# Optimization experiments

Hardware: AMD Instinct MI355X
Metric: run time of the kernel (lower is better)

The kernel has to match this reference:

```python
import jax, jax.numpy as jnp
import numpy as np

D_MODEL = 1024
N_HEADS = 16
FACTOR = 2
KEY_DIM = D_MODEL // N_HEADS            # 64
HEAD_DIM = D_MODEL * FACTOR // N_HEADS  # 128
SCALING = KEY_DIM ** -0.5
BSZ, SEQ = 2, 2048


def _rel_pos(slen):
    # angle: 1/10000**linspace(0,1,key_dim//2), each value repeated twice
    half = jnp.asarray(1.0) / jnp.power(10000.0, jnp.linspace(0.0, 1.0, KEY_DIM // 2))
    angle = jnp.repeat(half, 2)                              # [key_dim]
    decay = jnp.log(1.0 - 2.0 ** (-5.0 - jnp.arange(N_HEADS, dtype=jnp.float32)))  # [h], negative
    idx = jnp.arange(slen, dtype=jnp.float32)
    sin = jnp.sin(idx[:, None] * angle[None, :])             # [s, key_dim]
    cos = jnp.cos(idx[:, None] * angle[None, :])
    diff = idx[:, None] - idx[None, :]                       # [s, s]
    tril = diff >= 0
    mask = jnp.where(tril[None], jnp.exp(diff[None] * decay[:, None, None]), 0.0)  # [h, s, s]
    mask = mask / jnp.sqrt(mask.sum(axis=-1, keepdims=True))
    return sin, cos, mask


def _rotate_every_two(x):
    x1 = x[..., ::2]
    x2 = x[..., 1::2]
    return jnp.stack((-x2, x1), axis=-1).reshape(x.shape)


def _theta_shift(x, sin, cos):
    return x * cos + _rotate_every_two(x) * sin


def setup_inputs() -> dict:
    key = jax.random.key(0)
    ks = jax.random.split(key, 11)
    s = 1.0 / np.sqrt(D_MODEL)
    s2 = 1.0 / np.sqrt(D_MODEL * FACTOR)
    return {
        "x": jax.random.normal(ks[0], (BSZ, SEQ, D_MODEL), jnp.float32),
        "q_w": jax.random.uniform(ks[1], (D_MODEL, D_MODEL), jnp.float32, -s, s),
        "q_b": jax.random.uniform(ks[2], (D_MODEL,), jnp.float32, -s, s),
        "k_w": jax.random.uniform(ks[3], (D_MODEL, D_MODEL), jnp.float32, -s, s),
        "k_b": jax.random.uniform(ks[4], (D_MODEL,), jnp.float32, -s, s),
        "v_w": jax.random.uniform(ks[5], (D_MODEL, D_MODEL * FACTOR), jnp.float32, -s, s),
        "v_b": jax.random.uniform(ks[6], (D_MODEL * FACTOR,), jnp.float32, -s, s),
        "g_w": jax.random.uniform(ks[7], (D_MODEL, D_MODEL * FACTOR), jnp.float32, -s, s),
        "g_b": jax.random.uniform(ks[8], (D_MODEL * FACTOR,), jnp.float32, -s, s),
        "o_w": jax.random.uniform(ks[9], (D_MODEL * FACTOR, D_MODEL), jnp.float32, -s2, s2),
        "o_b": jax.random.uniform(ks[10], (D_MODEL,), jnp.float32, -s2, s2),
    }


def _forward(x, q_w, q_b, k_w, k_b, v_w, v_b, g_w, g_b, o_w, o_b):
    bsz, slen, _ = x.shape
    sin, cos, mask = _rel_pos(slen)
    q = x @ q_w + q_b
    k = (x @ k_w + k_b) * SCALING
    v = x @ v_w + v_b
    g = x @ g_w + g_b
    # [b, h, s, key_dim]
    q = q.reshape(bsz, slen, N_HEADS, KEY_DIM).transpose(0, 2, 1, 3)
    k = k.reshape(bsz, slen, N_HEADS, KEY_DIM).transpose(0, 2, 1, 3)
    qr = _theta_shift(q, sin, cos)
    kr = _theta_shift(k, sin, cos)
    vr = v.reshape(bsz, slen, N_HEADS, HEAD_DIM).transpose(0, 2, 1, 3)  # [b,h,s,head_dim]
    qk = jnp.einsum('bhmd,bhnd->bhmn', qr, kr) * mask                  # decay-masked scores
    denom = jnp.clip(jnp.abs(jax.lax.stop_gradient(qk).sum(axis=-1, keepdims=True)), 1.0, None)
    qk = qk / denom
    out = jnp.einsum('bhmn,bhnd->bhmd', qk, vr).transpose(0, 2, 1, 3)  # [b,s,h,head_dim]
    # per-head LayerNorm over head_dim, no affine
    mu = out.mean(axis=-1, keepdims=True)
    var = out.var(axis=-1, keepdims=True)
    out = (out - mu) / jnp.sqrt(var + 1e-5)
    out = out.reshape(bsz, slen, N_HEADS * HEAD_DIM)
    out = jax.nn.silu(g) * out
    return out @ o_w + o_b


def reference(x, q_w, q_b, k_w, k_b, v_w, v_b, g_w, g_b, o_w, o_b):
    return _forward(x, q_w, q_b, k_w, k_b, v_w, v_b, g_w, g_b, o_w, o_b)
```

## Files before the change

kernel.cpp:

```cpp
#include <hip/hip_runtime.h>
#include <hip/hip_bf16.h>


typedef __hip_bfloat16 bf16;
typedef short bf16x4 __attribute__((ext_vector_type(4)));
typedef short bf16x8 __attribute__((ext_vector_type(8)));
typedef float floatx4 __attribute__((ext_vector_type(4)));

#define B_SZ 2
#define SEQ 2048
#define NH 16
#define KD 64
#define HD 128

#define ASYNC16(gp, lp)                                                             \
  __builtin_amdgcn_global_load_lds(                                                 \
      (const __attribute__((address_space(1))) unsigned int*)(unsigned long long)(const void*)(gp), \
      (__attribute__((address_space(3))) unsigned int*)(unsigned int)(unsigned long long)(void*)(lp), \
      16, 0, 0)

__device__ __forceinline__ float b2f(bf16 x) { return __bfloat162float(x); }
__device__ __forceinline__ bf16 f2b(float x) { return __float2bfloat16(x); }

#define MFMA16(a, bb, c) __builtin_amdgcn_mfma_f32_16x16x32_bf16(a, bb, c, 0, 0, 0)

__global__ void convert_k(const float* __restrict__ in, bf16* __restrict__ out) {
  int i = blockIdx.x * 256 + threadIdx.x;
  float4 v = reinterpret_cast<const float4*>(in)[i];
  union { bf16 h[4]; bf16x4 v4; } u;
  u.h[0] = f2b(v.x); u.h[1] = f2b(v.y); u.h[2] = f2b(v.z); u.h[3] = f2b(v.w);
  reinterpret_cast<bf16x4*>(out)[i] = u.v4;
}

__global__ void transpose_k(const float* __restrict__ in, bf16* __restrict__ out,
                            int K, int N) {
  __shared__ float tile[32][33];
  int tx = threadIdx.x, ty = threadIdx.y;
  int n0 = blockIdx.x * 32, k0 = blockIdx.y * 32;
#pragma unroll
  for (int j = 0; j < 4; ++j)
    tile[ty + j * 8][tx] = in[(size_t)(k0 + ty + j * 8) * N + n0 + tx];
  __syncthreads();
#pragma unroll
  for (int j = 0; j < 4; ++j)
    out[(size_t)(n0 + ty + j * 8) * K + k0 + tx] = f2b(tile[tx][ty + j * 8]);
}

__global__ void vtrans_k(const bf16* __restrict__ in, bf16* __restrict__ out) {
  __shared__ bf16 tile[32][72];
  int tx = threadIdx.x, ty = threadIdx.y;
  int s0 = blockIdx.x * 32, c0 = blockIdx.y * 64, bz = blockIdx.z;
  const bf16* src = in + (size_t)bz * 2048 * 2048;
#pragma unroll
  for (int j = 0; j < 4; ++j) {
    int sr = ty + j * 8;
    tile[sr][tx] = src[(size_t)(s0 + sr) * 2048 + c0 + tx];
    tile[sr][tx + 32] = src[(size_t)(s0 + sr) * 2048 + c0 + 32 + tx];
  }
  __syncthreads();
  int tid = ty * 32 + tx;
  int dl = tid & 63, srun = tid >> 6;
  int c = c0 + dl, hh = c >> 7, d = c & 127;
  int dt = d >> 4, lw = d & 15;
  union { bf16 e[8]; bf16x8 v; } pk;
#pragma unroll
  for (int k = 0; k < 8; ++k) pk.e[k] = tile[srun * 8 + k][dl];
  size_t bh = (size_t)bz * NH + hh;
  int nt = s0 >> 5;
  size_t idx = ((bh * 64 + nt) * 8 + dt) * 512 + (size_t)(srun * 16 + lw) * 8;
  *(bf16x8*)&out[idx] = pk.v;
}

template <int BM, int BN, int KDIM, int MODE>
__global__ __launch_bounds__(256, 2) void gemm_bt(
    const bf16* __restrict__ A, const bf16* __restrict__ Bt, int Ndim,
    const float* __restrict__ bias_q, const float* __restrict__ bias_k,
    const float* __restrict__ bias_v, const float* __restrict__ bias_g,
    float* __restrict__ outCqk, bf16* __restrict__ out_v,
    float* __restrict__ out_g, float* __restrict__ outF) {
  __shared__ bf16 As[BM * 32];
  __shared__ bf16 Bs[BN * 32];
  const int tid = threadIdx.x;
  const int wave = tid >> 6, lane = tid & 63;
  const int quad = lane >> 4, l16 = lane & 15;
  const int m0 = blockIdx.y * BM, n0 = blockIdx.x * BN;
  constexpr int FI = BM / 32;
  constexpr int FJ = BN / 32;
  const int wm = (wave >> 1) * (BM / 2), wn = (wave & 1) * (BN / 2);

  floatx4 acc[FI][FJ] = {};

  for (int k0 = 0; k0 < KDIM; k0 += 32) {
#pragma unroll
    for (int j = 0; j < BM / 64; ++j) {
      int cbase = (j * 4 + wave) * 64;
      int c = cbase + lane;
      const bf16* g = A + (size_t)(m0 + (c >> 2)) * KDIM + k0 + (c & 3) * 8;
      ASYNC16(g, &As[cbase * 8]);
    }
#pragma unroll
    for (int j = 0; j < BN / 64; ++j) {
      int cbase = (j * 4 + wave) * 64;
      int c = cbase + lane;
      const bf16* g = Bt + (size_t)(n0 + (c >> 2)) * KDIM + k0 + (c & 3) * 8;
      ASYNC16(g, &Bs[cbase * 8]);
    }
    __syncthreads();

    bf16x8 af[FI], bfr[FJ];
#pragma unroll
    for (int i = 0; i < FI; ++i)
      af[i] = *(const bf16x8*)&As[(wm + i * 16 + l16) * 32 + quad * 8];
#pragma unroll
    for (int j = 0; j < FJ; ++j)
      bfr[j] = *(const bf16x8*)&Bs[(wn + j * 16 + l16) * 32 + quad * 8];
#pragma unroll
    for (int i = 0; i < FI; ++i)
#pragma unroll
      for (int j = 0; j < FJ; ++j)
        acc[i][j] = MFMA16(af[i], bfr[j], acc[i][j]);
    __syncthreads();
  }

#pragma unroll
  for (int i = 0; i < FI; ++i) {
#pragma unroll
    for (int j = 0; j < FJ; ++j) {
#pragma unroll
      for (int r = 0; r < 4; ++r) {
        int gm = m0 + wm + i * 16 + quad * 4 + r;
        int gn = n0 + wn + j * 16 + l16;
        float v = acc[i][j][r];
        if (MODE == 1) {
          v += bias_q[gn];
          outF[(size_t)gm * Ndim + gn] = v;
        } else {
          if (gn < 2048) {
            bool is_k = gn >= 1024;
            int jj = is_k ? gn - 1024 : gn;
            v += is_k ? bias_k[jj] : bias_q[jj];
            if (is_k) v *= 0.125f;
            outCqk[(size_t)gm * 2048 + gn] = v;
          } else if (gn < 4096) {
            int jj = gn - 2048;
            v += bias_v[jj];
            out_v[(size_t)gm * 2048 + jj] = f2b(v);
          } else {
            int jj = gn - 4096;
            v += bias_g[jj];
            out_g[(size_t)gm * 2048 + jj] = v;
          }
        }
      }
    }
  }
}

__global__ void router_k(const float* __restrict__ Cqk,
                         bf16* __restrict__ qh, bf16* __restrict__ ql,
                         bf16* __restrict__ kh, bf16* __restrict__ kl) {
  int t = blockIdx.x * 256 + threadIdx.x;
  int row = t >> 10, pc = t & 1023;
  int b = row >> 11, s = row & 2047;
  bool is_k = pc >= 512;
  int jj = (pc - (is_k ? 512 : 0)) * 2;
  int h = jj >> 6, d = jj & 63, ii = d >> 1;
  float2 v = *(const float2*)&Cqk[(size_t)row * 2048 + pc * 2];
  float half = exp2f(-(float)ii * (13.287712379549449f / 31.0f));
  float ang = (float)s * half;
  float sn = sinf(ang), cs = cosf(ang);
  float e = v.x * cs - v.y * sn;
  float o = v.y * cs + v.x * sn;
  bf16 eh = f2b(e), oh = f2b(o);
  bf16 el = f2b(e - b2f(eh)), ol = f2b(o - b2f(oh));
  size_t idx = (((size_t)b * NH + h) * SEQ + s) * KD + d;
  bf16* ph = is_k ? kh : qh;
  bf16* pl = is_k ? kl : ql;
  union { bf16 h2[2]; unsigned u; } uh, ul;
  uh.h2[0] = eh; uh.h2[1] = oh;
  ul.h2[0] = el; ul.h2[1] = ol;
  *(unsigned*)&ph[idx] = uh.u;
  *(unsigned*)&pl[idx] = ul.u;
}

__global__ __launch_bounds__(128, 2) void retention_k(
    const bf16* __restrict__ qh, const bf16* __restrict__ ql,
    const bf16* __restrict__ kh, const bf16* __restrict__ kl,
    const bf16* __restrict__ vf, const float* __restrict__ g,
    bf16* __restrict__ gated) {
  __shared__ bf16 KHs[2][32 * 64];
  __shared__ bf16 KLs[2][32 * 64];
  const int tid = threadIdx.x;
  const int wave = tid >> 6, lane = tid & 63;
  const int quad = lane >> 4, l16 = lane & 15;
  const int bid = blockIdx.x;
  const int px_raw = bid & 31;
  const int seg = bid >> 5;
  const int h = seg & 15, b = seg >> 4;
  const int px = ((seg >> 3) & 1) ? (31 - px_raw) : px_raw;
  const int bh = b * NH + h;
  const int bt_h = 63 - px;
  const int bt_l = px;
  const int m0h = bt_h * 32 + wave * 16;
  const int m0l = bt_l * 32 + wave * 16;
  const int ntiles = bt_h + 1;
  const int lt_ntiles = bt_l + 1;

  const float t = exp2f(-(float)(5 + h));
  const float lng = log1pf(-t);
  const float log2g = lng * 1.44269504088896340736f;

  float rfh, rfl;
  {
    int mh = m0h + l16, ml = m0l + l16;
    rfh = exp2f((float)mh * log2g) *
          rsqrtf(-expm1f((float)(mh + 1) * lng) / t);
    rfl = exp2f((float)ml * log2g) *
          rsqrtf(-expm1f((float)(ml + 1) * lng) / t);
  }
  const float gstep = exp2f(-32.0f * log2g);
  float cfq[8];
#pragma unroll
  for (int i = 0; i < 8; ++i) {
    int hh = i >> 2, r = i & 3;
    cfq[i] = exp2f(-(float)(hh * 16 + quad * 4 + r) * log2g);
  }

  const size_t qoffh = ((size_t)bh * SEQ + m0h + l16) * KD;
  const size_t qoffl = ((size_t)bh * SEQ + m0l + l16) * KD;
  bf16x8 aq0h_h = *(const bf16x8*)&qh[qoffh + quad * 8];
  bf16x8 aq1h_h = *(const bf16x8*)&qh[qoffh + 32 + quad * 8];
  bf16x8 aq0l_h = *(const bf16x8*)&ql[qoffh + quad * 8];
  bf16x8 aq1l_h = *(const bf16x8*)&ql[qoffh + 32 + quad * 8];
  bf16x8 aq0h_l = *(const bf16x8*)&qh[qoffl + quad * 8];
  bf16x8 aq1h_l = *(const bf16x8*)&qh[qoffl + 32 + quad * 8];
  bf16x8 aq0l_l = *(const bf16x8*)&ql[qoffl + quad * 8];
  bf16x8 aq1l_l = *(const bf16x8*)&ql[qoffl + 32 + quad * 8];

  floatx4 oacch[8] = {}, oaccl[8] = {};
  float rsh = 0.f, rsl = 0.f;

  const bf16* khb = kh + (size_t)bh * SEQ * KD;
  const bf16* klb = kl + (size_t)bh * SEQ * KD;
  const bf16* vfb = vf + (size_t)bh * 64 * 8 * 512;
  const int lo8 = lane * 8;

  auto stage = [&](int nt, int buf) {
    const int n0s = nt * 32;
#pragma unroll
    for (int j = 0; j < 4; ++j) {
      int cc = wave * 4 + j;
      const bf16* src = (cc < 4) ? khb : klb;
      bf16* dst = (cc < 4) ? KHs[buf] : KLs[buf];
      int r = ((cc & 3) * 8) + (lane >> 3);
      int s = lane & 7;
      int q = (s - r) & 7;
      ASYNC16(src + (size_t)(n0s + r) * KD + q * 8, &dst[(cc & 3) * 512]);
    }
  };

  auto buildPA = [&](const floatx4* sc, float rf, float& rs, int n0,
                     int m0) -> bf16x8 {
    const int m = m0 + l16;
    const bool full = (m0 >= n0 + 31);
    unsigned d[4];
#pragma unroll
    for (int hh = 0; hh < 2; ++hh) {
      float p[4];
#pragma unroll
      for (int r = 0; r < 4; ++r) {
        float pv;
        if (full) {
          pv = sc[hh][r] * rf * cfq[hh * 4 + r];
        } else {
          int n = n0 + hh * 16 + quad * 4 + r;
          pv = (m >= n) ? sc[hh][r] * rf * cfq[hh * 4 + r] : 0.f;
        }
        rs += pv;
        p[r] = pv;
      }
      union { bf16 hx[2]; unsigned u; } u0, u1;
      u0.hx[0] = f2b(p[0]); u0.hx[1] = f2b(p[1]);
      u1.hx[0] = f2b(p[2]); u1.hx[1] = f2b(p[3]);
      d[hh * 2 + 0] = u0.u;
      d[hh * 2 + 1] = u1.u;
    }
    unsigned a0 = d[0], b0 = d[2];
    asm("v_permlane32_swap_b32 %0, %1" : "+v"(a0), "+v"(b0));
    asm("v_permlane16_swap_b32 %0, %1" : "+v"(a0), "+v"(b0));
    unsigned a1 = d[1], b1 = d[3];
    asm("v_permlane32_swap_b32 %0, %1" : "+v"(a1), "+v"(b1));
    asm("v_permlane16_swap_b32 %0, %1" : "+v"(a1), "+v"(b1));
    union { unsigned u[4]; bf16x8 v; } pu;
    pu.u[0] = a0; pu.u[1] = a1; pu.u[2] = b0; pu.u[3] = b1;
    return pu.v;
  };

  stage(0, 0);
  for (int nt = 0; nt < ntiles; ++nt) {
    const int n0 = nt * 32;
    const int cur = nt & 1;
    asm volatile("s_waitcnt vmcnt(0) lgkmcnt(0)" ::: "memory");
    __syncthreads();

    bf16x8 vv[8];
#pragma unroll
    for (int c = 0; c < 8; ++c)
      vv[c] = *(const bf16x8*)(vfb + ((size_t)nt * 8 + c) * 512 + lo8);

    {
      int pf = (nt + 1 < ntiles) ? nt + 1 : nt;
      stage(pf, cur ^ 1);
    }

    const bool hact = (n0 <= m0h + 15);
    const bool lact = (n0 <= m0l + 15);

    floatx4 sch[2], scl[2];
#pragma unroll
    for (int hh = 0; hh < 2; ++hh) {
      int krow = hh * 16 + l16;
      int c0 = ((quad + krow) & 7) * 8;
      int c1 = ((quad + 4 + krow) & 7) * 8;
      bf16x8 bkh0 = *(const bf16x8*)&KHs[cur][krow * 64 + c0];
      bf16x8 bkh1 = *(const bf16x8*)&KHs[cur][krow * 64 + c1];
      bf16x8 bkl0 = *(const bf16x8*)&KLs[cur][krow * 64 + c0];
      bf16x8 bkl1 = *(const bf16x8*)&KLs[cur][krow * 64 + c1];
      if (hact) {
        floatx4 z1 = {0.f, 0.f, 0.f, 0.f}, z2 = z1, z3 = z1;
        z1 = MFMA16(bkh0, aq0h_h, z1);
        z2 = MFMA16(bkh0, aq0l_h, z2);
        z3 = MFMA16(bkl0, aq0h_h, z3);
        z1 = MFMA16(bkh1, aq1h_h, z1);
        z2 = MFMA16(bkh1, aq1l_h, z2);
        z3 = MFMA16(bkl1, aq1h_h, z3);
        sch[hh] = z1 + z2 + z3;
      }
      if (lact) {
        floatx4 z1 = {0.f, 0.f, 0.f, 0.f}, z2 = z1, z3 = z1;
        z1 = MFMA16(bkh0, aq0h_l, z1);
        z2 = MFMA16(bkh0, aq0l_l, z2);
        z3 = MFMA16(bkl0, aq0h_l, z3);
        z1 = MFMA16(bkh1, aq1h_l, z1);
        z2 = MFMA16(bkh1, aq1l_l, z2);
        z3 = MFMA16(bkl1, aq1h_l, z3);
        scl[hh] = z1 + z2 + z3;
      }
    }

    bf16x8 pah, pal;
    if (hact) pah = buildPA(sch, rfh, rsh, n0, m0h);
    if (lact) pal = buildPA(scl, rfl, rsl, n0, m0l);
    rfh *= gstep;
    if (nt + 1 < lt_ntiles) rfl *= gstep;

#pragma unroll
    for (int dt = 0; dt < 8; ++dt) {
      if (hact) oacch[dt] = MFMA16(pah, vv[dt], oacch[dt]);
      if (lact) oaccl[dt] = MFMA16(pal, vv[dt], oaccl[dt]);
    }
  }

  auto finalize = [&](floatx4* oacc, float rowsum, int m0) {
    float v = rowsum;
    v += __shfl_xor(v, 16);
    v += __shfl_xor(v, 32);
    float inv_den[4];
#pragma unroll
    for (int r = 0; r < 4; ++r) {
      float dsum = __shfl(v, quad * 4 + r);
      inv_den[r] = 1.0f / fmaxf(fabsf(dsum), 1.0f);
    }
    float s1[4] = {}, s2[4] = {};
#pragma unroll
    for (int dt = 0; dt < 8; ++dt) {
#pragma unroll
      for (int r = 0; r < 4; ++r) {
        float vv2 = oacc[dt][r] * inv_den[r];
        oacc[dt][r] = vv2;
        s1[r] += vv2;
        s2[r] += vv2 * vv2;
      }
    }
    float mean[4], istd[4];
#pragma unroll
    for (int r = 0; r < 4; ++r) {
      float a = s1[r], q2 = s2[r];
      a += __shfl_xor(a, 1); a += __shfl_xor(a, 2);
      a += __shfl_xor(a, 4); a += __shfl_xor(a, 8);
      q2 += __shfl_xor(q2, 1); q2 += __shfl_xor(q2, 2);
      q2 += __shfl_xor(q2, 4); q2 += __shfl_xor(q2, 8);
      mean[r] = a * (1.0f / 128.0f);
      float var = q2 * (1.0f / 128.0f) - mean[r] * mean[r];
      istd[r] = rsqrtf(fmaxf(var, 0.0f) + 1e-5f);
    }
#pragma unroll
    for (int dt = 0; dt < 8; ++dt) {
#pragma unroll
      for (int r = 0; r < 4; ++r) {
        int m = m0 + quad * 4 + r;
        int col = h * HD + dt * 16 + l16;
        float vv2 = (oacc[dt][r] - mean[r]) * istd[r];
        float gv = g[((size_t)b * SEQ + m) * 2048 + col];
        float sg = gv / (1.0f + expf(-gv));
        gated[((size_t)b * SEQ + m) * 2048 + col] = f2b(sg * vv2);
      }
    }
  };
  finalize(oacch, rsh, m0h);
  finalize(oaccl, rsl, m0l);
}

extern "C" void kernel_launch(void* const* d_in, const int* in_sizes, int n_in,
                              void* d_out, int out_size, void* d_ws,
                              size_t ws_size, hipStream_t stream) {
  const float* x   = (const float*)d_in[0];
  const float* q_w = (const float*)d_in[1];
  const float* q_b = (const float*)d_in[2];
  const float* k_w = (const float*)d_in[3];
  const float* k_b = (const float*)d_in[4];
  const float* v_w = (const float*)d_in[5];
  const float* v_b = (const float*)d_in[6];
  const float* g_w = (const float*)d_in[7];
  const float* g_b = (const float*)d_in[8];
  const float* o_w = (const float*)d_in[9];
  const float* o_b = (const float*)d_in[10];

  char* ws = (char*)d_ws;
  bf16* Wt    = (bf16*)ws; ws += (size_t)6144 * 1024 * 2;
  bf16* oT    = (bf16*)ws; ws += (size_t)1024 * 2048 * 2;
  bf16* xb    = (bf16*)ws; ws += (size_t)4096 * 1024 * 2;
  float* Cqk  = (float*)ws; ws += (size_t)4096 * 2048 * 4;
  bf16* qhb   = (bf16*)ws; ws += (size_t)32 * 2048 * 64 * 2;
  bf16* qlb   = (bf16*)ws; ws += (size_t)32 * 2048 * 64 * 2;
  bf16* khb   = (bf16*)ws; ws += (size_t)32 * 2048 * 64 * 2;
  bf16* klb   = (bf16*)ws; ws += (size_t)32 * 2048 * 64 * 2;
  bf16* vfb   = (bf16*)ws; ws += (size_t)32 * 64 * 8 * 512 * 2;
  float* gbuf = (float*)ws; ws += (size_t)2 * 2048 * 2048 * 4;
  bf16* gated = (bf16*)ws; ws += (size_t)4096 * 2048 * 2;
  bf16* vbuf  = gated;

  convert_k<<<(4096 * 1024 / 4) / 256, 256, 0, stream>>>(x, xb);

  dim3 tb(32, 8);
  transpose_k<<<dim3(1024 / 32, 1024 / 32), tb, 0, stream>>>(q_w, Wt, 1024, 1024);
  transpose_k<<<dim3(1024 / 32, 1024 / 32), tb, 0, stream>>>(k_w, Wt + (size_t)1024 * 1024, 1024, 1024);
  transpose_k<<<dim3(2048 / 32, 1024 / 32), tb, 0, stream>>>(v_w, Wt + (size_t)2048 * 1024, 1024, 2048);
  transpose_k<<<dim3(2048 / 32, 1024 / 32), tb, 0, stream>>>(g_w, Wt + (size_t)4096 * 1024, 1024, 2048);
  transpose_k<<<dim3(1024 / 32, 2048 / 32), tb, 0, stream>>>(o_w, oT, 2048, 1024);

  gemm_bt<128, 128, 1024, 0><<<dim3(6144 / 128, 4096 / 128), 256, 0, stream>>>(
      xb, Wt, 6144, q_b, k_b, v_b, g_b, Cqk, vbuf, gbuf, nullptr);

  vtrans_k<<<dim3(2048 / 32, 2048 / 64, B_SZ), tb, 0, stream>>>(vbuf, vfb);

  router_k<<<(4096 * 1024) / 256, 256, 0, stream>>>(Cqk, qhb, qlb, khb, klb);

  retention_k<<<dim3(1024), 128, 0, stream>>>(
      qhb, qlb, khb, klb, vfb, gbuf, gated);

  gemm_bt<128, 64, 2048, 1><<<dim3(1024 / 64, 4096 / 128), 256, 0, stream>>>(
      gated, oT, 1024, o_b, nullptr, nullptr, nullptr, nullptr, nullptr,
      nullptr, (float*)d_out);
}
```

Before: 341.3 us.

## Pre-swizzle K into MFMA fragment layout and load directly to registers

The router kernel now writes K (high and low bf16 parts) in a per-tile fragment layout that matches the MFMA operand order, the same way V is already stored. The retention kernel drops its LDS double buffer, its async global-to-LDS copies and its per-tile __syncthreads, and each wave loads its K fragments straight from global memory into registers. Those loads are software-pipelined one tile ahead using two register sets. This removes LDS traffic and block-wide barriers, but each of the two waves now loads K on its own, and the extra registers may hurt occupancy under launch_bounds(128,2).

```diff
diff --git a/kernel.cpp b/kernel.cpp
--- a/kernel.cpp
+++ b/kernel.cpp
@@ -158,7 +158,7 @@
 
 __global__ void router_k(const float* __restrict__ Cqk,
                          bf16* __restrict__ qh, bf16* __restrict__ ql,
-                         bf16* __restrict__ kh, bf16* __restrict__ kl) {
+                         bf16* __restrict__ kf) {
   int t = blockIdx.x * 256 + threadIdx.x;
   int row = t >> 10, pc = t & 1023;
   int b = row >> 11, s = row & 2047;
@@ -173,23 +173,28 @@
   float o = v.y * cs + v.x * sn;
   bf16 eh = f2b(e), oh = f2b(o);
   bf16 el = f2b(e - b2f(eh)), ol = f2b(o - b2f(oh));
-  size_t idx = (((size_t)b * NH + h) * SEQ + s) * KD + d;
-  bf16* ph = is_k ? kh : qh;
-  bf16* pl = is_k ? kl : ql;
   union { bf16 h2[2]; unsigned u; } uh, ul;
   uh.h2[0] = eh; uh.h2[1] = oh;
   ul.h2[0] = el; ul.h2[1] = ol;
-  *(unsigned*)&ph[idx] = uh.u;
-  *(unsigned*)&pl[idx] = ul.u;
+  size_t bh = (size_t)b * NH + h;
+  if (!is_k) {
+    size_t idx = (bh * SEQ + s) * KD + d;
+    *(unsigned*)&qh[idx] = uh.u;
+    *(unsigned*)&ql[idx] = ul.u;
+  } else {
+    int nt = s >> 5, hh = (s >> 4) & 1, lr = s & 15;
+    int dh = d >> 5, qd = (d >> 3) & 3, jb = d & 7;
+    size_t cbase = ((bh * 64 + nt) * 8);
+    size_t off = (size_t)(qd * 16 + lr) * 8 + jb;
+    *(unsigned*)&kf[(cbase + hh * 2 + dh) * 512 + off] = uh.u;
+    *(unsigned*)&kf[(cbase + 4 + hh * 2 + dh) * 512 + off] = ul.u;
+  }
 }
 
 __global__ __launch_bounds__(128, 2) void retention_k(
     const bf16* __restrict__ qh, const bf16* __restrict__ ql,
-    const bf16* __restrict__ kh, const bf16* __restrict__ kl,
-    const bf16* __restrict__ vf, const float* __restrict__ g,
-    bf16* __restrict__ gated) {
-  __shared__ bf16 KHs[2][32 * 64];
-  __shared__ bf16 KLs[2][32 * 64];
+    const bf16* __restrict__ kf, const bf16* __restrict__ vf,
+    const float* __restrict__ g, bf16* __restrict__ gated) {
   const int tid = threadIdx.x;
   const int wave = tid >> 6, lane = tid & 63;
   const int quad = lane >> 4, l16 = lane & 15;
@@ -240,23 +245,15 @@
   floatx4 oacch[8] = {}, oaccl[8] = {};
   float rsh = 0.f, rsl = 0.f;
 
-  const bf16* khb = kh + (size_t)bh * SEQ * KD;
-  const bf16* klb = kl + (size_t)bh * SEQ * KD;
+  const bf16* kfb = kf + (size_t)bh * 64 * 8 * 512;
   const bf16* vfb = vf + (size_t)bh * 64 * 8 * 512;
   const int lo8 = lane * 8;
 
-  auto stage = [&](int nt, int buf) {
-    const int n0s = nt * 32;
-#pragma unroll
-    for (int j = 0; j < 4; ++j) {
-      int cc = wave * 4 + j;
-      const bf16* src = (cc < 4) ? khb : klb;
-      bf16* dst = (cc < 4) ? KHs[buf] : KLs[buf];
-      int r = ((cc & 3) * 8) + (lane >> 3);
-      int s = lane & 7;
-      int q = (s - r) & 7;
-      ASYNC16(src + (size_t)(n0s + r) * KD + q * 8, &dst[(cc & 3) * 512]);
-    }
+  bf16x8 kA[8], kB[8];
+  auto loadK = [&](bf16x8 (&d)[8], int nt_) {
+#pragma unroll
+    for (int c = 0; c < 8; ++c)
+      d[c] = *(const bf16x8*)(kfb + ((size_t)nt_ * 8 + c) * 512 + lo8);
   };
 
   auto buildPA = [&](const floatx4* sc, float rf, float& rs, int n0,
@@ -296,36 +293,21 @@
     return pu.v;
   };
 
-  stage(0, 0);
-  for (int nt = 0; nt < ntiles; ++nt) {
+  auto body = [&](bf16x8 (&k)[8], int nt) {
     const int n0 = nt * 32;
-    const int cur = nt & 1;
-    asm volatile("s_waitcnt vmcnt(0) lgkmcnt(0)" ::: "memory");
-    __syncthreads();
-
     bf16x8 vv[8];
 #pragma unroll
     for (int c = 0; c < 8; ++c)
       vv[c] = *(const bf16x8*)(vfb + ((size_t)nt * 8 + c) * 512 + lo8);
 
-    {
-      int pf = (nt + 1 < ntiles) ? nt + 1 : nt;
-      stage(pf, cur ^ 1);
-    }
-
     const bool hact = (n0 <= m0h + 15);
     const bool lact = (n0 <= m0l + 15);
 
     floatx4 sch[2], scl[2];
 #pragma unroll
     for (int hh = 0; hh < 2; ++hh) {
-      int krow = hh * 16 + l16;
-      int c0 = ((quad + krow) & 7) * 8;
-      int c1 = ((quad + 4 + krow) & 7) * 8;
-      bf16x8 bkh0 = *(const bf16x8*)&KHs[cur][krow * 64 + c0];
-      bf16x8 bkh1 = *(const bf16x8*)&KHs[cur][krow * 64 + c1];
-      bf16x8 bkl0 = *(const bf16x8*)&KLs[cur][krow * 64 + c0];
-      bf16x8 bkl1 = *(const bf16x8*)&KLs[cur][krow * 64 + c1];
+      bf16x8 bkh0 = k[hh * 2 + 0], bkh1 = k[hh * 2 + 1];
+      bf16x8 bkl0 = k[4 + hh * 2 + 0], bkl1 = k[4 + hh * 2 + 1];
       if (hact) {
         floatx4 z1 = {0.f, 0.f, 0.f, 0.f}, z2 = z1, z3 = z1;
         z1 = MFMA16(bkh0, aq0h_h, z1);
@@ -359,6 +341,17 @@
       if (hact) oacch[dt] = MFMA16(pah, vv[dt], oacch[dt]);
       if (lact) oaccl[dt] = MFMA16(pal, vv[dt], oaccl[dt]);
     }
+  };
+
+  loadK(kA, 0);
+  int nt = 0;
+  while (true) {
+    if (nt + 1 < ntiles) loadK(kB, nt + 1);
+    body(kA, nt);
+    if (++nt >= ntiles) break;
+    if (nt + 1 < ntiles) loadK(kA, nt + 1);
+    body(kB, nt);
+    if (++nt >= ntiles) break;
   }
 
   auto finalize = [&](floatx4* oacc, float rowsum, int m0) {
@@ -433,8 +426,7 @@
   float* Cqk  = (float*)ws; ws += (size_t)4096 * 2048 * 4;
   bf16* qhb   = (bf16*)ws; ws += (size_t)32 * 2048 * 64 * 2;
   bf16* qlb   = (bf16*)ws; ws += (size_t)32 * 2048 * 64 * 2;
-  bf16* khb   = (bf16*)ws; ws += (size_t)32 * 2048 * 64 * 2;
-  bf16* klb   = (bf16*)ws; ws += (size_t)32 * 2048 * 64 * 2;
+  bf16* kfb   = (bf16*)ws; ws += (size_t)32 * 64 * 8 * 512 * 2;
   bf16* vfb   = (bf16*)ws; ws += (size_t)32 * 64 * 8 * 512 * 2;
   float* gbuf = (float*)ws; ws += (size_t)2 * 2048 * 2048 * 4;
   bf16* gated = (bf16*)ws; ws += (size_t)4096 * 2048 * 2;
@@ -454,10 +446,10 @@
 
   vtrans_k<<<dim3(2048 / 32, 2048 / 64, B_SZ), tb, 0, stream>>>(vbuf, vfb);
 
-  router_k<<<(4096 * 1024) / 256, 256, 0, stream>>>(Cqk, qhb, qlb, khb, klb);
+  router_k<<<(4096 * 1024) / 256, 256, 0, stream>>>(Cqk, qhb, qlb, kfb);
 
   retention_k<<<dim3(1024), 128, 0, stream>>>(
-      qhb, qlb, khb, klb, vfb, gbuf, gated);
+      qhb, qlb, kfb, vfb, gbuf, gated);
 
   gemm_bt<128, 64, 2048, 1><<<dim3(1024 / 64, 4096 / 128), 256, 0, stream>>>(
       gated, oT, 1024, o_b, nullptr, nullptr, nullptr, nullptr, nullptr,
```

After: 357.5 us. +4.7%, slower.
